# Kernel tuning notes

Measured on AMD Instinct MI355X. Metric: run time of the kernel, lower is better.

The kernel has to match this reference:

```python
import jax, jax.numpy as jnp
import numpy as np

TOP_K = 2
NUM_EXPERTS = 8
D_MODEL = 1024


def setup_inputs() -> dict:
    key = jax.random.key(0)
    kx, kw, kb = jax.random.split(key, 3)
    x = jax.random.normal(kx, (8, 4096, D_MODEL), dtype=jnp.float32)
    bound = 1.0 / np.sqrt(D_MODEL)
    W = jax.random.uniform(kw, (NUM_EXPERTS, D_MODEL), dtype=jnp.float32, minval=-bound, maxval=bound)
    b = jax.random.uniform(kb, (NUM_EXPERTS,), dtype=jnp.float32, minval=-bound, maxval=bound)
    return {"x": x, "W": W, "b": b}


def reference(x, W, b):
    # logits: [B, S, E]
    logits = jnp.einsum('bsd,ed->bse', x, W) + b
    values, indices = jax.lax.top_k(logits, TOP_K)  # [B,S,K]
    # softmax over a tensor that is -inf everywhere except top-k positions
    # == softmax over the top-k values, scattered back; non-selected experts get 0.
    topk_w = jax.nn.softmax(values, axis=-1)  # [B,S,K]
    one_hot = jax.nn.one_hot(indices, NUM_EXPERTS, dtype=logits.dtype)  # [B,S,K,E]
    weights = jnp.einsum('bsk,bske->bse', topk_w, one_hot)
    return weights, indices
```

## Files before the change

### kernel.cpp

```cpp
#include <hip/hip_runtime.h>
#include <math.h>

#define D_MODEL 1024
#define NUM_EXPERTS 8
#define TOP_K 2
#define LANES_PER_TOKEN 8
#define TOKENS_PER_WAVE 8
#define WAVES_PER_BLOCK 4
#define TOKENS_PER_BLOCK (TOKENS_PER_WAVE * WAVES_PER_BLOCK)

typedef float f4 __attribute__((ext_vector_type(4)));

__global__ __launch_bounds__(256) void gating_kernel(
    const float* __restrict__ x, const float* __restrict__ W,
    const float* __restrict__ b, float* __restrict__ out_w,
    float* __restrict__ out_idx, int n_tokens)
{
    __shared__ float Wlds[NUM_EXPERTS * D_MODEL];

    {
        const f4* Wg = (const f4*)W;
        f4* Ws = (f4*)Wlds;
        const int tid = threadIdx.x;
#pragma unroll
        for (int i = 0; i < (NUM_EXPERTS * D_MODEL / 4) / 256; ++i)
            Ws[tid + i * 256] = Wg[tid + i * 256];
    }
    __syncthreads();

    const int wave = threadIdx.x >> 6;
    const int lane = threadIdx.x & 63;
    const int g = lane >> 3;
    const int l = lane & 7;
    const int token = blockIdx.x * TOKENS_PER_BLOCK + wave * TOKENS_PER_WAVE + g;
    if (token >= n_tokens) return;

    const f4* xg = (const f4*)x + (size_t)token * (D_MODEL / 4) + l;
    const f4* Wl = (const f4*)Wlds + l;

    float acc[NUM_EXPERTS];
#pragma unroll
    for (int e = 0; e < NUM_EXPERTS; ++e) acc[e] = 0.f;

#pragma unroll
    for (int c = 0; c < 4; ++c) {
        f4 xa[8];
#pragma unroll
        for (int kk = 0; kk < 8; ++kk)
            xa[kk] = __builtin_nontemporal_load(xg + (c * 8 + kk) * 8);
#pragma unroll
        for (int e = 0; e < NUM_EXPERTS; ++e) {
            float s = acc[e];
#pragma unroll
            for (int kk = 0; kk < 8; ++kk) {
                const f4 wv = Wl[e * 256 + (c * 8 + kk) * 8];
                s += xa[kk].x * wv.x + xa[kk].y * wv.y +
                     xa[kk].z * wv.z + xa[kk].w * wv.w;
            }
            acc[e] = s;
        }
    }

#pragma unroll
    for (int e = 0; e < NUM_EXPERTS; ++e) {
        float v = acc[e];
        v += __shfl_xor(v, 1, 64);
        v += __shfl_xor(v, 2, 64);
        v += __shfl_xor(v, 4, 64);
        acc[e] = v + b[e];
    }

    float v0 = -INFINITY, v1 = -INFINITY;
    int i0 = 0, i1 = 0;
#pragma unroll
    for (int e = 0; e < NUM_EXPERTS; ++e) {
        float v = acc[e];
        if (v > v0) { v1 = v0; i1 = i0; v0 = v; i0 = e; }
        else if (v > v1) { v1 = v; i1 = e; }
    }
    const float e1 = expf(v1 - v0);
    const float w0 = 1.f / (1.f + e1);
    const float w1 = e1 * w0;

    if (l < 2) {
        const int base = l * 4;
        f4 v4;
        v4.x = (base + 0 == i0) ? w0 : ((base + 0 == i1) ? w1 : 0.f);
        v4.y = (base + 1 == i0) ? w0 : ((base + 1 == i1) ? w1 : 0.f);
        v4.z = (base + 2 == i0) ? w0 : ((base + 2 == i1) ? w1 : 0.f);
        v4.w = (base + 3 == i0) ? w0 : ((base + 3 == i1) ? w1 : 0.f);
        ((f4*)(out_w + (size_t)token * NUM_EXPERTS))[l] = v4;
    } else if (l == 2) {
        *(float2*)(out_idx + (size_t)token * TOP_K) =
            make_float2((float)i0, (float)i1);
    }
}

extern "C" void kernel_launch(void* const* d_in, const int* in_sizes, int n_in,
                              void* d_out, int out_size, void* d_ws, size_t ws_size,
                              hipStream_t stream) {
    const float* x = (const float*)d_in[0];
    const float* W = (const float*)d_in[1];
    const float* b = (const float*)d_in[2];
    float* out = (float*)d_out;

    const int n_tokens = in_sizes[0] / D_MODEL;
    float* out_w   = out;
    float* out_idx = out + (size_t)n_tokens * NUM_EXPERTS;

    const int grid = (n_tokens + TOKENS_PER_BLOCK - 1) / TOKENS_PER_BLOCK;
    gating_kernel<<<grid, 256, 0, stream>>>(x, W, b, out_w, out_idx, n_tokens);
}
```

Measured before the change: 185.7 us.

## Keep gate weights in registers and process tokens per wave with prefetch

Drops the shared-memory staging of W. Each lane now holds its slice of all 8 expert rows in registers (128 floats), and a whole wave computes one token at a time across the full d_model. Per-token dot products are reduced with DPP, swizzle and permlane32 cross-lane ops. The next token's x is double-buffered to overlap loads with compute. This removes the LDS fill and barrier per block, but adds 48 cross-lane reduction steps per token and higher register pressure, which may cut occupancy on a memory-bound kernel.

```diff
diff --git a/kernel.cpp b/kernel.cpp
--- a/kernel.cpp
+++ b/kernel.cpp
@@ -4,95 +4,122 @@
 #define D_MODEL 1024
 #define NUM_EXPERTS 8
 #define TOP_K 2
-#define LANES_PER_TOKEN 8
 #define TOKENS_PER_WAVE 8
 #define WAVES_PER_BLOCK 4
 #define TOKENS_PER_BLOCK (TOKENS_PER_WAVE * WAVES_PER_BLOCK)
 
 typedef float f4 __attribute__((ext_vector_type(4)));
 
+template<int CTRL>
+__device__ __forceinline__ float dpp_add(float v) {
+    int s = __builtin_amdgcn_update_dpp(0, __builtin_bit_cast(int, v),
+                                        CTRL, 0xF, 0xF, true);
+    return v + __builtin_bit_cast(float, s);
+}
+
+__device__ __forceinline__ float wave_sum64(float v) {
+    v = dpp_add<0xB1>(v);
+    v = dpp_add<0x4E>(v);
+    v = dpp_add<0x141>(v);
+    v = dpp_add<0x140>(v);
+    int t = __builtin_amdgcn_ds_swizzle(__builtin_bit_cast(int, v), 0x401F);
+    v += __builtin_bit_cast(float, t);
+#if __has_builtin(__builtin_amdgcn_permlane32_swap)
+    {
+        unsigned a = __builtin_bit_cast(unsigned, v);
+        auto p = __builtin_amdgcn_permlane32_swap(a, a, false, false);
+        v = __builtin_bit_cast(float, (unsigned)p[0]) +
+            __builtin_bit_cast(float, (unsigned)p[1]);
+    }
+#else
+    v += __shfl_xor(v, 32, 64);
+#endif
+    return v;
+}
+
+__device__ __forceinline__ float dot4(f4 a, f4 b) {
+    return a.x * b.x + a.y * b.y + a.z * b.z + a.w * b.w;
+}
+
 __global__ __launch_bounds__(256) void gating_kernel(
     const float* __restrict__ x, const float* __restrict__ W,
     const float* __restrict__ b, float* __restrict__ out_w,
     float* __restrict__ out_idx, int n_tokens)
 {
-    __shared__ float Wlds[NUM_EXPERTS * D_MODEL];
-
-    {
-        const f4* Wg = (const f4*)W;
-        f4* Ws = (f4*)Wlds;
-        const int tid = threadIdx.x;
-#pragma unroll
-        for (int i = 0; i < (NUM_EXPERTS * D_MODEL / 4) / 256; ++i)
-            Ws[tid + i * 256] = Wg[tid + i * 256];
-    }
-    __syncthreads();
-
     const int wave = threadIdx.x >> 6;
     const int lane = threadIdx.x & 63;
-    const int g = lane >> 3;
-    const int l = lane & 7;
-    const int token = blockIdx.x * TOKENS_PER_BLOCK + wave * TOKENS_PER_WAVE + g;
-    if (token >= n_tokens) return;
+    const int wid = blockIdx.x * WAVES_PER_BLOCK + wave;
+    const int token0 = wid * TOKENS_PER_WAVE;
+    if (token0 >= n_tokens) return;
+    const int nt = (n_tokens - token0 < TOKENS_PER_WAVE) ? (n_tokens - token0)
+                                                         : TOKENS_PER_WAVE;
 
-    const f4* xg = (const f4*)x + (size_t)token * (D_MODEL / 4) + l;
-    const f4* Wl = (const f4*)Wlds + l;
+    f4 Wr[NUM_EXPERTS][4];
+    {
+        const f4* Wg = (const f4*)W + lane;
+#pragma unroll
+        for (int e = 0; e < NUM_EXPERTS; ++e)
+#pragma unroll
+            for (int i = 0; i < 4; ++i)
+                Wr[e][i] = Wg[e * 256 + i * 64];
+    }
+    const f4 blo = ((const f4*)b)[0];
+    const f4 bhi = ((const f4*)b)[1];
+    const float bb[NUM_EXPERTS] = {blo.x, blo.y, blo.z, blo.w,
+                                   bhi.x, bhi.y, bhi.z, bhi.w};
 
-    float acc[NUM_EXPERTS];
+    const f4* xw = (const f4*)x + (size_t)token0 * (D_MODEL / 4) + lane;
+
+    f4 xs[2][4];
 #pragma unroll
-    for (int e = 0; e < NUM_EXPERTS; ++e) acc[e] = 0.f;
+    for (int i = 0; i < 4; ++i)
+        xs[0][i] = __builtin_nontemporal_load(xw + i * 64);
 
 #pragma unroll
-    for (int c = 0; c < 4; ++c) {
-        f4 xa[8];
+    for (int t = 0; t < TOKENS_PER_WAVE; ++t) {
+        const int cur = t & 1;
+        const int nxt = cur ^ 1;
+        if (t + 1 < nt) {
 #pragma unroll
-        for (int kk = 0; kk < 8; ++kk)
-            xa[kk] = __builtin_nontemporal_load(xg + (c * 8 + kk) * 8);
+            for (int i = 0; i < 4; ++i)
+                xs[nxt][i] =
+                    __builtin_nontemporal_load(xw + (t + 1) * 256 + i * 64);
+        }
+        if (t >= nt) break;
+
+        float acc[NUM_EXPERTS];
 #pragma unroll
         for (int e = 0; e < NUM_EXPERTS; ++e) {
-            float s = acc[e];
+            float s = dot4(xs[cur][0], Wr[e][0]) + dot4(xs[cur][1], Wr[e][1]) +
+                      dot4(xs[cur][2], Wr[e][2]) + dot4(xs[cur][3], Wr[e][3]);
+            acc[e] = wave_sum64(s) + bb[e];
+        }
+
+        float v0 = -INFINITY, v1 = -INFINITY;
+        int i0 = 0, i1 = 0;
 #pragma unroll
-            for (int kk = 0; kk < 8; ++kk) {
-                const f4 wv = Wl[e * 256 + (c * 8 + kk) * 8];
-                s += xa[kk].x * wv.x + xa[kk].y * wv.y +
-                     xa[kk].z * wv.z + xa[kk].w * wv.w;
-            }
-            acc[e] = s;
+        for (int e = 0; e < NUM_EXPERTS; ++e) {
+            float v = acc[e];
+            if (v > v0) { v1 = v0; i1 = i0; v0 = v; i0 = e; }
+            else if (v > v1) { v1 = v; i1 = e; }
         }
-    }
+        const float e1 = expf(v1 - v0);
+        const float w0 = 1.f / (1.f + e1);
+        const float w1 = e1 * w0;
 
-#pragma unroll
-    for (int e = 0; e < NUM_EXPERTS; ++e) {
-        float v = acc[e];
-        v += __shfl_xor(v, 1, 64);
-        v += __shfl_xor(v, 2, 64);
-        v += __shfl_xor(v, 4, 64);
-        acc[e] = v + b[e];
-    }
-
-    float v0 = -INFINITY, v1 = -INFINITY;
-    int i0 = 0, i1 = 0;
-#pragma unroll
-    for (int e = 0; e < NUM_EXPERTS; ++e) {
-        float v = acc[e];
-        if (v > v0) { v1 = v0; i1 = i0; v0 = v; i0 = e; }
-        else if (v > v1) { v1 = v; i1 = e; }
-    }
-    const float e1 = expf(v1 - v0);
-    const float w0 = 1.f / (1.f + e1);
-    const float w1 = e1 * w0;
-
-    if (l < 2) {
-        const int base = l * 4;
-        f4 v4;
-        v4.x = (base + 0 == i0) ? w0 : ((base + 0 == i1) ? w1 : 0.f);
-        v4.y = (base + 1 == i0) ? w0 : ((base + 1 == i1) ? w1 : 0.f);
-        v4.z = (base + 2 == i0) ? w0 : ((base + 2 == i1) ? w1 : 0.f);
-        v4.w = (base + 3 == i0) ? w0 : ((base + 3 == i1) ? w1 : 0.f);
-        ((f4*)(out_w + (size_t)token * NUM_EXPERTS))[l] = v4;
-    } else if (l == 2) {
-        *(float2*)(out_idx + (size_t)token * TOP_K) =
-            make_float2((float)i0, (float)i1);
+        const size_t token = (size_t)(token0 + t);
+        if (lane < 2) {
+            const int base = lane * 4;
+            f4 v4;
+            v4.x = (base + 0 == i0) ? w0 : ((base + 0 == i1) ? w1 : 0.f);
+            v4.y = (base + 1 == i0) ? w0 : ((base + 1 == i1) ? w1 : 0.f);
+            v4.z = (base + 2 == i0) ? w0 : ((base + 2 == i1) ? w1 : 0.f);
+            v4.w = (base + 3 == i0) ? w0 : ((base + 3 == i1) ? w1 : 0.f);
+            ((f4*)(out_w + token * NUM_EXPERTS))[lane] = v4;
+        } else if (lane == 2) {
+            *(float2*)(out_idx + token * TOP_K) =
+                make_float2((float)i0, (float)i1);
+        }
     }
 }
 
```

Result: slower. 191.2 us (+3.0%).

## Process two tokens per lane group with double-buffered x loads and DPP reductions

Applied to the files above, without the earlier changes.

Each 8-lane group now handles two tokens, so every LDS read of W feeds two dot products, and the block covers twice as many tokens. The first x chunk is loaded before the W copy into LDS, and later chunks are double-buffered so global loads overlap the FMA work. Cross-lane shuffles are replaced by DPP adds, and the bias is read as two vector loads. The grid is halved and register use grows from the doubled x buffers, which may lower occupancy.

```diff
diff --git a/kernel.cpp b/kernel.cpp
--- a/kernel.cpp
+++ b/kernel.cpp
@@ -5,11 +5,24 @@
 #define NUM_EXPERTS 8
 #define TOP_K 2
 #define LANES_PER_TOKEN 8
-#define TOKENS_PER_WAVE 8
+#define GROUPS_PER_WAVE 8
+#define TOKENS_PER_GROUP 2
+#define TOKENS_PER_WAVE (GROUPS_PER_WAVE * TOKENS_PER_GROUP)
 #define WAVES_PER_BLOCK 4
 #define TOKENS_PER_BLOCK (TOKENS_PER_WAVE * WAVES_PER_BLOCK)
 
 typedef float f4 __attribute__((ext_vector_type(4)));
+
+template<int CTRL>
+__device__ __forceinline__ float dpp_add(float v) {
+    int s = __builtin_amdgcn_update_dpp(0, __builtin_bit_cast(int, v),
+                                        CTRL, 0xF, 0xF, true);
+    return v + __builtin_bit_cast(float, s);
+}
+
+__device__ __forceinline__ float dot4(f4 a, f4 b) {
+    return a.x * b.x + a.y * b.y + a.z * b.z + a.w * b.w;
+}
 
 __global__ __launch_bounds__(256) void gating_kernel(
     const float* __restrict__ x, const float* __restrict__ W,
@@ -17,6 +30,26 @@
     float* __restrict__ out_idx, int n_tokens)
 {
     __shared__ float Wlds[NUM_EXPERTS * D_MODEL];
+
+    const int wave = threadIdx.x >> 6;
+    const int lane = threadIdx.x & 63;
+    const int g = lane >> 3;
+    const int l = lane & 7;
+    const int base = blockIdx.x * TOKENS_PER_BLOCK + wave * TOKENS_PER_WAVE;
+    const int t0 = base + g;
+    const int t1 = base + 8 + g;
+
+    const int t0c = t0 < n_tokens ? t0 : 0;
+    const int t1c = t1 < n_tokens ? t1 : 0;
+    const f4* xg0 = (const f4*)x + (size_t)t0c * (D_MODEL / 4) + l;
+    const f4* xg1 = (const f4*)x + (size_t)t1c * (D_MODEL / 4) + l;
+
+    f4 xa[2][TOKENS_PER_GROUP][8];
+#pragma unroll
+    for (int kk = 0; kk < 8; ++kk) {
+        xa[0][0][kk] = __builtin_nontemporal_load(xg0 + kk * 8);
+        xa[0][1][kk] = __builtin_nontemporal_load(xg1 + kk * 8);
+    }
 
     {
         const f4* Wg = (const f4*)W;
@@ -28,71 +61,79 @@
     }
     __syncthreads();
 
-    const int wave = threadIdx.x >> 6;
-    const int lane = threadIdx.x & 63;
-    const int g = lane >> 3;
-    const int l = lane & 7;
-    const int token = blockIdx.x * TOKENS_PER_BLOCK + wave * TOKENS_PER_WAVE + g;
-    if (token >= n_tokens) return;
-
-    const f4* xg = (const f4*)x + (size_t)token * (D_MODEL / 4) + l;
     const f4* Wl = (const f4*)Wlds + l;
 
-    float acc[NUM_EXPERTS];
+    float acc[TOKENS_PER_GROUP][NUM_EXPERTS];
 #pragma unroll
-    for (int e = 0; e < NUM_EXPERTS; ++e) acc[e] = 0.f;
+    for (int tt = 0; tt < TOKENS_PER_GROUP; ++tt)
+#pragma unroll
+        for (int e = 0; e < NUM_EXPERTS; ++e) acc[tt][e] = 0.f;
 
 #pragma unroll
     for (int c = 0; c < 4; ++c) {
-        f4 xa[8];
+        const int cur = c & 1, nxt = cur ^ 1;
+        if (c < 3) {
 #pragma unroll
-        for (int kk = 0; kk < 8; ++kk)
-            xa[kk] = __builtin_nontemporal_load(xg + (c * 8 + kk) * 8);
+            for (int kk = 0; kk < 8; ++kk) {
+                xa[nxt][0][kk] =
+                    __builtin_nontemporal_load(xg0 + ((c + 1) * 8 + kk) * 8);
+                xa[nxt][1][kk] =
+                    __builtin_nontemporal_load(xg1 + ((c + 1) * 8 + kk) * 8);
+            }
+        }
 #pragma unroll
         for (int e = 0; e < NUM_EXPERTS; ++e) {
-            float s = acc[e];
+            float s0 = acc[0][e];
+            float s1 = acc[1][e];
 #pragma unroll
             for (int kk = 0; kk < 8; ++kk) {
                 const f4 wv = Wl[e * 256 + (c * 8 + kk) * 8];
-                s += xa[kk].x * wv.x + xa[kk].y * wv.y +
-                     xa[kk].z * wv.z + xa[kk].w * wv.w;
+                s0 += dot4(xa[cur][0][kk], wv);
+                s1 += dot4(xa[cur][1][kk], wv);
             }
-            acc[e] = s;
+            acc[0][e] = s0;
+            acc[1][e] = s1;
         }
     }
 
+    const f4 blo = ((const f4*)b)[0];
+    const f4 bhi = ((const f4*)b)[1];
+    const float bb[NUM_EXPERTS] = {blo.x, blo.y, blo.z, blo.w,
+                                   bhi.x, bhi.y, bhi.z, bhi.w};
+
 #pragma unroll
-    for (int e = 0; e < NUM_EXPERTS; ++e) {
-        float v = acc[e];
-        v += __shfl_xor(v, 1, 64);
-        v += __shfl_xor(v, 2, 64);
-        v += __shfl_xor(v, 4, 64);
-        acc[e] = v + b[e];
-    }
+    for (int tt = 0; tt < TOKENS_PER_GROUP; ++tt) {
+        const int token = base + tt * 8 + g;
+        if (token >= n_tokens) continue;
 
-    float v0 = -INFINITY, v1 = -INFINITY;
-    int i0 = 0, i1 = 0;
+        float v0 = -INFINITY, v1 = -INFINITY;
+        int i0 = 0, i1 = 0;
 #pragma unroll
-    for (int e = 0; e < NUM_EXPERTS; ++e) {
-        float v = acc[e];
-        if (v > v0) { v1 = v0; i1 = i0; v0 = v; i0 = e; }
-        else if (v > v1) { v1 = v; i1 = e; }
-    }
-    const float e1 = expf(v1 - v0);
-    const float w0 = 1.f / (1.f + e1);
-    const float w1 = e1 * w0;
+        for (int e = 0; e < NUM_EXPERTS; ++e) {
+            float v = acc[tt][e];
+            v = dpp_add<0xB1>(v);
+            v = dpp_add<0x4E>(v);
+            v = dpp_add<0x141>(v);
+            v += bb[e];
+            if (v > v0) { v1 = v0; i1 = i0; v0 = v; i0 = e; }
+            else if (v > v1) { v1 = v; i1 = e; }
+        }
+        const float e1 = expf(v1 - v0);
+        const float w0 = 1.f / (1.f + e1);
+        const float w1 = e1 * w0;
 
-    if (l < 2) {
-        const int base = l * 4;
-        f4 v4;
-        v4.x = (base + 0 == i0) ? w0 : ((base + 0 == i1) ? w1 : 0.f);
-        v4.y = (base + 1 == i0) ? w0 : ((base + 1 == i1) ? w1 : 0.f);
-        v4.z = (base + 2 == i0) ? w0 : ((base + 2 == i1) ? w1 : 0.f);
-        v4.w = (base + 3 == i0) ? w0 : ((base + 3 == i1) ? w1 : 0.f);
-        ((f4*)(out_w + (size_t)token * NUM_EXPERTS))[l] = v4;
-    } else if (l == 2) {
-        *(float2*)(out_idx + (size_t)token * TOP_K) =
-            make_float2((float)i0, (float)i1);
+        if (l < 2) {
+            const int bd = l * 4;
+            f4 v4;
+            v4.x = (bd + 0 == i0) ? w0 : ((bd + 0 == i1) ? w1 : 0.f);
+            v4.y = (bd + 1 == i0) ? w0 : ((bd + 1 == i1) ? w1 : 0.f);
+            v4.z = (bd + 2 == i0) ? w0 : ((bd + 2 == i1) ? w1 : 0.f);
+            v4.w = (bd + 3 == i0) ? w0 : ((bd + 3 == i1) ? w1 : 0.f);
+            ((f4*)(out_w + (size_t)token * NUM_EXPERTS))[l] = v4;
+        } else if (l == 2) {
+            *(float2*)(out_idx + (size_t)token * TOP_K) =
+                make_float2((float)i0, (float)i1);
+        }
     }
 }
 
```

New measurement: 528.0 us. +184.3%, slower.

## Transpose x tiles through swizzled LDS so each lane owns one token

Applied to the files above, without the earlier changes.

Replaces the 8-lanes-per-token scheme (W staged in LDS, cross-lane shuffle reduction) with one-wave blocks where each lane computes a full token. Coalesced x loads are double-buffered in registers and transposed through an XOR-swizzled LDS tile. W is read directly from global memory as wave-uniform loads. This drops the per-block 32KB W staging, the barrier and the shuffle reduction, and makes output stores per lane. In exchange it relies on scalar/cached W reads, runs without explicit barriers between the LDS writes and reads within the single wave, and has a long serial per-lane dot product.

```diff
diff --git a/kernel.cpp b/kernel.cpp
--- a/kernel.cpp
+++ b/kernel.cpp
@@ -4,77 +4,89 @@
 #define D_MODEL 1024
 #define NUM_EXPERTS 8
 #define TOP_K 2
-#define LANES_PER_TOKEN 8
-#define TOKENS_PER_WAVE 8
-#define WAVES_PER_BLOCK 4
-#define TOKENS_PER_BLOCK (TOKENS_PER_WAVE * WAVES_PER_BLOCK)
+#define TOKENS_PER_BLOCK 64
 
 typedef float f4 __attribute__((ext_vector_type(4)));
 
-__global__ __launch_bounds__(256) void gating_kernel(
+__global__ __launch_bounds__(64) void gating_kernel(
     const float* __restrict__ x, const float* __restrict__ W,
     const float* __restrict__ b, float* __restrict__ out_w,
     float* __restrict__ out_idx, int n_tokens)
 {
-    __shared__ float Wlds[NUM_EXPERTS * D_MODEL];
+    __shared__ float xt[TOKENS_PER_BLOCK * 64];
 
-    {
-        const f4* Wg = (const f4*)W;
-        f4* Ws = (f4*)Wlds;
-        const int tid = threadIdx.x;
+    const int lane = threadIdx.x;
+    const int base = blockIdx.x * TOKENS_PER_BLOCK;
+    const int g = lane >> 3;
+    const int h = lane >> 4;
+    const int q16 = lane & 15;
+
+    int rowoff[16];
 #pragma unroll
-        for (int i = 0; i < (NUM_EXPERTS * D_MODEL / 4) / 256; ++i)
-            Ws[tid + i * 256] = Wg[tid + i * 256];
+    for (int j = 0; j < 16; ++j) {
+        int r = base + 4 * j + h;
+        if (r >= n_tokens) r = n_tokens - 1;
+        rowoff[j] = r * (D_MODEL / 4) + q16;
     }
-    __syncthreads();
 
-    const int wave = threadIdx.x >> 6;
-    const int lane = threadIdx.x & 63;
-    const int g = lane >> 3;
-    const int l = lane & 7;
-    const int token = blockIdx.x * TOKENS_PER_BLOCK + wave * TOKENS_PER_WAVE + g;
-    if (token >= n_tokens) return;
+    f4* xtf = (f4*)xt;
+    const f4* xg = (const f4*)x;
+    const f4* Wf = (const f4*)W;
 
-    const f4* xg = (const f4*)x + (size_t)token * (D_MODEL / 4) + l;
-    const f4* Wl = (const f4*)Wlds + l;
+    int wslot[16];
+#pragma unroll
+    for (int j = 0; j < 16; ++j)
+        wslot[j] = (4 * j + h) * 16 + (q16 ^ (j >> 1));
+    int rslot[16];
+#pragma unroll
+    for (int s = 0; s < 16; ++s)
+        rslot[s] = lane * 16 + (s ^ g);
 
     float acc[NUM_EXPERTS];
 #pragma unroll
     for (int e = 0; e < NUM_EXPERTS; ++e) acc[e] = 0.f;
 
+    f4 xa[16];
 #pragma unroll
-    for (int c = 0; c < 4; ++c) {
-        f4 xa[8];
+    for (int j = 0; j < 16; ++j)
+        xa[j] = __builtin_nontemporal_load(xg + rowoff[j]);
+
+#pragma unroll 1
+    for (int c = 0; c < 16; ++c) {
 #pragma unroll
-        for (int kk = 0; kk < 8; ++kk)
-            xa[kk] = __builtin_nontemporal_load(xg + (c * 8 + kk) * 8);
+        for (int j = 0; j < 16; ++j)
+            xtf[wslot[j]] = xa[j];
+
+        if (c < 15) {
 #pragma unroll
-        for (int e = 0; e < NUM_EXPERTS; ++e) {
-            float s = acc[e];
+            for (int j = 0; j < 16; ++j)
+                xa[j] = __builtin_nontemporal_load(
+                    xg + rowoff[j] + (c + 1) * 16);
+        }
+
 #pragma unroll
-            for (int kk = 0; kk < 8; ++kk) {
-                const f4 wv = Wl[e * 256 + (c * 8 + kk) * 8];
-                s += xa[kk].x * wv.x + xa[kk].y * wv.y +
-                     xa[kk].z * wv.z + xa[kk].w * wv.w;
+        for (int s = 0; s < 16; ++s) {
+            const f4 xv = xtf[rslot[s]];
+#pragma unroll
+            for (int e = 0; e < NUM_EXPERTS; ++e) {
+                const f4 wv = Wf[e * 256 + c * 16 + s];
+                acc[e] += xv.x * wv.x + xv.y * wv.y +
+                          xv.z * wv.z + xv.w * wv.w;
             }
-            acc[e] = s;
         }
     }
 
-#pragma unroll
-    for (int e = 0; e < NUM_EXPERTS; ++e) {
-        float v = acc[e];
-        v += __shfl_xor(v, 1, 64);
-        v += __shfl_xor(v, 2, 64);
-        v += __shfl_xor(v, 4, 64);
-        acc[e] = v + b[e];
-    }
+    const f4 bl = ((const f4*)b)[0];
+    const f4 bh = ((const f4*)b)[1];
+    const float lg[NUM_EXPERTS] = {
+        acc[0] + bl.x, acc[1] + bl.y, acc[2] + bl.z, acc[3] + bl.w,
+        acc[4] + bh.x, acc[5] + bh.y, acc[6] + bh.z, acc[7] + bh.w};
 
     float v0 = -INFINITY, v1 = -INFINITY;
     int i0 = 0, i1 = 0;
 #pragma unroll
     for (int e = 0; e < NUM_EXPERTS; ++e) {
-        float v = acc[e];
+        const float v = lg[e];
         if (v > v0) { v1 = v0; i1 = i0; v0 = v; i0 = e; }
         else if (v > v1) { v1 = v; i1 = e; }
     }
@@ -82,15 +94,20 @@
     const float w0 = 1.f / (1.f + e1);
     const float w1 = e1 * w0;
 
-    if (l < 2) {
-        const int base = l * 4;
-        f4 v4;
-        v4.x = (base + 0 == i0) ? w0 : ((base + 0 == i1) ? w1 : 0.f);
-        v4.y = (base + 1 == i0) ? w0 : ((base + 1 == i1) ? w1 : 0.f);
-        v4.z = (base + 2 == i0) ? w0 : ((base + 2 == i1) ? w1 : 0.f);
-        v4.w = (base + 3 == i0) ? w0 : ((base + 3 == i1) ? w1 : 0.f);
-        ((f4*)(out_w + (size_t)token * NUM_EXPERTS))[l] = v4;
-    } else if (l == 2) {
+    const int token = base + lane;
+    if (token < n_tokens) {
+        f4 wlo, whi;
+        wlo.x = (0 == i0) ? w0 : ((0 == i1) ? w1 : 0.f);
+        wlo.y = (1 == i0) ? w0 : ((1 == i1) ? w1 : 0.f);
+        wlo.z = (2 == i0) ? w0 : ((2 == i1) ? w1 : 0.f);
+        wlo.w = (3 == i0) ? w0 : ((3 == i1) ? w1 : 0.f);
+        whi.x = (4 == i0) ? w0 : ((4 == i1) ? w1 : 0.f);
+        whi.y = (5 == i0) ? w0 : ((5 == i1) ? w1 : 0.f);
+        whi.z = (6 == i0) ? w0 : ((6 == i1) ? w1 : 0.f);
+        whi.w = (7 == i0) ? w0 : ((7 == i1) ? w1 : 0.f);
+        f4* po = (f4*)(out_w + (size_t)token * NUM_EXPERTS);
+        po[0] = wlo;
+        po[1] = whi;
         *(float2*)(out_idx + (size_t)token * TOP_K) =
             make_float2((float)i0, (float)i1);
     }
@@ -109,5 +126,5 @@
     float* out_idx = out + (size_t)n_tokens * NUM_EXPERTS;
 
     const int grid = (n_tokens + TOKENS_PER_BLOCK - 1) / TOKENS_PER_BLOCK;
-    gating_kernel<<<grid, 256, 0, stream>>>(x, W, b, out_w, out_idx, n_tokens);
+    gating_kernel<<<grid, 64, 0, stream>>>(x, W, b, out_w, out_idx, n_tokens);
 }
```

Result: slower. 276.6 us (+48.9%).
